# Kernel tuning notes

Measured on AMD Instinct MI355X. Metric: run time of the kernel, lower is better.

The kernel has to match this reference:

```python
import jax, jax.numpy as jnp
import numpy as np

B, NS, NT = 4, 512, 512
D_IN, C1, R, C2 = 128, 64, 32, 32
E = 32768
STEPS = 10


def setup_inputs() -> dict:
    key = jax.random.key(0)
    ks = jax.random.split(key, 12)
    inp = {}
    inp['x_s'] = jax.random.normal(ks[0], (B * NS, D_IN), jnp.float32)
    inp['edge_index_s'] = jax.random.randint(ks[1], (2, E), 0, B * NS, jnp.int32)
    inp['edge_attr_s'] = jax.random.uniform(ks[2], (E,), jnp.float32)
    inp['batch_s'] = (jnp.arange(B * NS, dtype=jnp.int32) // NS)
    inp['x_t'] = jax.random.normal(ks[3], (B * NT, D_IN), jnp.float32)
    inp['edge_index_t'] = jax.random.randint(ks[4], (2, E), 0, B * NT, jnp.int32)
    inp['edge_attr_t'] = jax.random.uniform(ks[5], (E,), jnp.float32)
    inp['batch_t'] = (jnp.arange(B * NT, dtype=jnp.int32) // NT)
    inp['W1'] = jax.random.normal(ks[6], (D_IN, C1), jnp.float32) / np.float32(np.sqrt(D_IN))
    inp['W2'] = jax.random.normal(ks[7], (R, C2), jnp.float32) / np.float32(np.sqrt(R))
    inp['mw1'] = jax.random.normal(ks[8], (C2, C2), jnp.float32) / np.float32(np.sqrt(C2))
    inp['mb1'] = jnp.zeros((C2,), jnp.float32)
    inp['mw2'] = jax.random.normal(ks[9], (C2, 1), jnp.float32) / np.float32(np.sqrt(C2))
    inp['mb2'] = jnp.zeros((1,), jnp.float32)
    inp['r'] = jax.random.normal(ks[10], (STEPS, B, NS, R), jnp.float32)
    return inp


def psi(x, src, dst, ea, W, n):
    # simple message-passing GNN: edge-weighted neighbor aggregation + linear + ReLU
    m = jax.ops.segment_sum(x[src] * ea[:, None], dst, num_segments=n)
    return jax.nn.relu((x + m) @ W)


def reference(x_s, edge_index_s, edge_attr_s, batch_s, x_t, edge_index_t, edge_attr_t,
              batch_t, W1, W2, mw1, mb1, mw2, mb2, r):
    # Uniform graph sizes -> to_dense_batch is a reshape and all masks are True,
    # so masked_softmax reduces to plain softmax; batch_s/batch_t kept for interface fidelity.
    ss, ds = edge_index_s[0], edge_index_s[1]
    st, dt = edge_index_t[0], edge_index_t[1]
    h_s = psi(x_s, ss, ds, edge_attr_s, W1, B * NS).reshape(B, NS, C1)
    h_t = psi(x_t, st, dt, edge_attr_t, W1, B * NT).reshape(B, NT, C1)
    S_hat0 = jnp.einsum('bsc,btc->bst', h_s, h_t)  # [B, NS, NT]
    S_0 = jax.nn.softmax(S_hat0, axis=-1)

    def step(S_hat, r_i):
        S = jax.nn.softmax(S_hat, axis=-1)
        r_t = jnp.einsum('bst,bsr->btr', S, r_i)  # S^T @ r_s
        o_s = psi(r_i.reshape(B * NS, R), ss, ds, edge_attr_s, W2, B * NS).reshape(B, NS, C2)
        o_t = psi(r_t.reshape(B * NT, R), st, dt, edge_attr_t, W2, B * NT).reshape(B, NT, C2)
        Dm = o_s[:, :, None, :] - o_t[:, None, :, :]  # [B, NS, NT, C2] outer difference
        upd = (jax.nn.relu(Dm @ mw1 + mb1) @ mw2 + mb2)[..., 0]
        return S_hat + upd, None

    S_hat, _ = jax.lax.scan(step, S_hat0, r)
    S_L = jax.nn.softmax(S_hat, axis=-1)
    return (S_0, S_L)
```

## Files before the change

### kernel.cpp

```cpp
#include <hip/hip_runtime.h>


constexpr int kB = 4;
constexpr int kNS = 512;
constexpr int kNT = 512;
constexpr int kDin = 128;
constexpr int kC1 = 64;
constexpr int kR = 32;
constexpr int kC2 = 32;
constexpr int kE = 32768;
constexpr int kSteps = 10;
constexpr int kN = kB * kNS;
constexpr int kChunkStride = kR * kN;

__global__ void k_hist(const int* __restrict__ ei_s, const int* __restrict__ ei_t,
                       int* __restrict__ deg) {
  int g = blockIdx.y;
  const int* dst = (g ? ei_t : ei_s) + kE;
  int e = blockIdx.x * 256 + threadIdx.x;
  atomicAdd(&deg[g * kN + dst[e]], 1);
}

__global__ void k_scan(const int* __restrict__ deg, int* __restrict__ off,
                       int* __restrict__ cur) {
  int g = blockIdx.x;
  const int* d = deg + g * kN;
  int* o = off + g * (kN + 1);
  int* c = cur + g * kN;
  __shared__ int sums[256];
  int tid = threadIdx.x;
  int loc[8];
  int s = 0;
#pragma unroll
  for (int i = 0; i < 8; ++i) { loc[i] = d[tid * 8 + i]; s += loc[i]; }
  sums[tid] = s;
  __syncthreads();
  for (int st = 1; st < 256; st <<= 1) {
    int v = (tid >= st) ? sums[tid - st] : 0;
    __syncthreads();
    sums[tid] += v;
    __syncthreads();
  }
  int base = (tid > 0) ? sums[tid - 1] : 0;
#pragma unroll
  for (int i = 0; i < 8; ++i) {
    int idx = tid * 8 + i;
    o[idx] = base;
    c[idx] = base;
    base += loc[i];
  }
  if (tid == 255) o[kN] = base;
}

__global__ void k_scatter(const int* __restrict__ ei_s, const int* __restrict__ ei_t,
                          const float* __restrict__ ea_s, const float* __restrict__ ea_t,
                          int* __restrict__ cur, int* __restrict__ srcs,
                          float* __restrict__ eaw) {
  int g = blockIdx.y;
  const int* ei = g ? ei_t : ei_s;
  const float* ea = g ? ea_t : ea_s;
  int e = blockIdx.x * 256 + threadIdx.x;
  int d = ei[kE + e];
  int srcv = ei[e];
  int pos = atomicAdd(&cur[g * kN + d], 1);
  srcs[g * kE + pos] = srcv;
  eaw[g * kE + pos] = ea[e];
}

__global__ __launch_bounds__(128) void k_psi1(
    const float* __restrict__ x_s, const float* __restrict__ x_t,
    const int* __restrict__ srcs, const float* __restrict__ eaw,
    const int* __restrict__ off, const float* __restrict__ W1, float* __restrict__ h) {
  int g = blockIdx.y;
  const float* x = g ? x_t : x_s;
  const int* sr = srcs + g * kE;
  const float* ew = eaw + g * kE;
  const int* o = off + g * (kN + 1);
  float* ho = h + (size_t)g * kN * kC1;
  int n = blockIdx.x, f = threadIdx.x;
  __shared__ float y[kDin];
  int beg = o[n], end = o[n + 1];
  float m = 0.f;
  for (int idx = beg; idx < end; ++idx)
    m += x[(size_t)sr[idx] * kDin + f] * ew[idx];
  y[f] = x[(size_t)n * kDin + f] + m;
  __syncthreads();
  if (f < kC1) {
    float acc = 0.f;
#pragma unroll 16
    for (int k = 0; k < kDin; ++k) acc += y[k] * W1[k * kC1 + f];
    ho[(size_t)n * kC1 + f] = fmaxf(acc, 0.f);
  }
}

__global__ __launch_bounds__(256) void k_shat0(const float* __restrict__ h,
                                               float* __restrict__ Shat,
                                               float* __restrict__ pstatm,
                                               float* __restrict__ pstatl) {
  int b = blockIdx.z, s0 = blockIdx.y * 64, t0 = blockIdx.x * 64;
  const float* hs = h + (size_t)(b * kNS + s0) * kC1;
  const float* ht = h + (size_t)kN * kC1 + (size_t)(b * kNT + t0) * kC1;
  __shared__ float As[64 * 68];
  __shared__ float Bs[64 * 68];
  int tid = threadIdx.x;
#pragma unroll
  for (int k2 = 0; k2 < 4; ++k2) {
    int idx = tid + k2 * 256;
    int row = idx >> 4, c4 = idx & 15;
    float4 va = *(const float4*)(hs + (size_t)row * kC1 + c4 * 4);
    *(float4*)&As[row * 68 + c4 * 4] = va;
    float4 vb = *(const float4*)(ht + (size_t)row * kC1 + c4 * 4);
    *(float4*)&Bs[row * 68 + c4 * 4] = vb;
  }
  __syncthreads();
  int ts = tid >> 4, tt = tid & 15;
  float acc[4][4] = {};
#pragma unroll
  for (int cc = 0; cc < 16; ++cc) {
    float4 a[4], bt[4];
#pragma unroll
    for (int i = 0; i < 4; ++i) a[i] = *(const float4*)&As[(ts * 4 + i) * 68 + cc * 4];
#pragma unroll
    for (int k = 0; k < 4; ++k) bt[k] = *(const float4*)&Bs[(tt + 16 * k) * 68 + cc * 4];
#pragma unroll
    for (int i = 0; i < 4; ++i)
#pragma unroll
      for (int k = 0; k < 4; ++k)
        acc[i][k] += a[i].x * bt[k].x + a[i].y * bt[k].y + a[i].z * bt[k].z + a[i].w * bt[k].w;
  }
#pragma unroll
  for (int i = 0; i < 4; ++i) {
    int s = s0 + ts * 4 + i;
    float* row = Shat + (size_t)(b * kNS + s) * kNT;
#pragma unroll
    for (int k = 0; k < 4; ++k) row[t0 + tt + 16 * k] = acc[i][k];
  }
#pragma unroll
  for (int i = 0; i < 4; ++i) {
    float mm = fmaxf(fmaxf(acc[i][0], acc[i][1]), fmaxf(acc[i][2], acc[i][3]));
#pragma unroll
    for (int o2 = 8; o2; o2 >>= 1) mm = fmaxf(mm, __shfl_xor(mm, o2, 64));
    float se = 0.f;
#pragma unroll
    for (int k = 0; k < 4; ++k) se += __expf(acc[i][k] - mm);
#pragma unroll
    for (int o2 = 8; o2; o2 >>= 1) se += __shfl_xor(se, o2, 64);
    if (tt == 0) {
      int grow = b * kNS + s0 + ts * 4 + i;
      pstatm[blockIdx.x * kN + grow] = mm;
      pstatl[blockIdx.x * kN + grow] = se;
    }
  }
}

__global__ __launch_bounds__(256) void k_rt(const float* __restrict__ Shat,
                                            const float* __restrict__ pstatm,
                                            const float* __restrict__ pstatl,
                                            const float* __restrict__ ri,
                                            float* __restrict__ part, int nc,
                                            float* __restrict__ Sout) {
  int b = blockIdx.z, cs = blockIdx.y, s0 = cs * 64, t0 = blockIdx.x * 32;
  __shared__ float Wt[64 * 32];
  __shared__ float rch[64 * 32];
  __shared__ float lm[64], ll[64];
  int tid = threadIdx.x;
  if (tid < 64) {
    int row = b * kNS + s0 + tid;
    float m = -3.4e38f;
    for (int c = 0; c < nc; ++c) m = fmaxf(m, pstatm[c * kN + row]);
    float l = 0.f;
    for (int c = 0; c < nc; ++c) l += __expf(pstatm[c * kN + row] - m) * pstatl[c * kN + row];
    lm[tid] = m;
    ll[tid] = 1.f / l;
  }
  __syncthreads();
#pragma unroll
  for (int k2 = 0; k2 < 2; ++k2) {
    int idx = tid + k2 * 256;
    int row = idx >> 3, c4 = idx & 7;
    int grow = b * kNS + s0 + row;
    float4 v = *(const float4*)(Shat + (size_t)grow * kNT + t0 + c4 * 4);
    float m = lm[row], l = ll[row];
    float4 wv;
    wv.x = __expf(v.x - m) * l;
    wv.y = __expf(v.y - m) * l;
    wv.z = __expf(v.z - m) * l;
    wv.w = __expf(v.w - m) * l;
    *(float4*)&Wt[row * 32 + c4 * 4] = wv;
    if (Sout) *(float4*)(Sout + (size_t)grow * kNT + t0 + c4 * 4) = wv;
    float4 rv = *(const float4*)(ri + (size_t)grow * kR + c4 * 4);
    *(float4*)&rch[row * 32 + c4 * 4] = rv;
  }
  __syncthreads();
  int t_l = tid & 31, jg = tid >> 5;
  float4 acc = make_float4(0.f, 0.f, 0.f, 0.f);
  for (int s = 0; s < 64; ++s) {
    float wv = Wt[s * 32 + t_l];
    float4 rv = *(const float4*)&rch[s * 32 + jg * 4];
    acc.x += wv * rv.x; acc.y += wv * rv.y; acc.z += wv * rv.z; acc.w += wv * rv.w;
  }
  int gcol = b * kNT + t0 + t_l;
  *(float4*)&part[(size_t)cs * kChunkStride + (size_t)gcol * kR + jg * 4] = acc;
}

__device__ __forceinline__ void psi2_node(
    int n, const float* __restrict__ vin, const int* __restrict__ sr,
    const float* __restrict__ ew, const int* __restrict__ o,
    const float* __restrict__ W2, const float* __restrict__ mw1,
    const float* __restrict__ mb1, float* __restrict__ Pout) {
  int lane = threadIdx.x & 63;
  int f = lane & 31, hh = lane >> 5;
  int beg = o[n], end = o[n + 1];
  float m = 0.f;
  for (int idx = beg + hh; idx < end; idx += 2)
    m += vin[(size_t)sr[idx] * kR + f] * ew[idx];
  m += __shfl_down(m, 32, 64);
  float v = vin[(size_t)n * kR + f] + m;
  float acc = 0.f;
#pragma unroll
  for (int k = 0; k < kC2; ++k) acc += __shfl(v, k, 64) * W2[k * kC2 + f];
  float ov = fmaxf(acc, 0.f);
  float p = mb1 ? mb1[f] : 0.f;
#pragma unroll
  for (int k = 0; k < kC2; ++k) p += __shfl(ov, k, 64) * mw1[k * kC2 + f];
  if (lane < 32) Pout[(size_t)n * kC2 + f] = p;
}

__global__ __launch_bounds__(256) void k_psi2s(
    const float* __restrict__ r, const int* __restrict__ srcs,
    const float* __restrict__ eaw, const int* __restrict__ off,
    const float* __restrict__ W2, const float* __restrict__ mw1,
    const float* __restrict__ mb1, float* __restrict__ PsAll) {
  int nn = blockIdx.x * 4 + (threadIdx.x >> 6);
  int step = nn >> 11, node = nn & (kN - 1);
  psi2_node(node, r + (size_t)step * kN * kR, srcs, eaw, off, W2, mw1, mb1,
            PsAll + (size_t)step * kN * kR);
}

__global__ __launch_bounds__(256) void k_psi2t(
    const float* __restrict__ part, const int* __restrict__ srcs,
    const float* __restrict__ eaw, const int* __restrict__ off,
    const float* __restrict__ W2, const float* __restrict__ mw1,
    float* __restrict__ Pt) {
  int n = blockIdx.x * 4 + (threadIdx.x >> 6);
  int lane = threadIdx.x & 63;
  int f = lane & 31, hh = lane >> 5;
  const int* sr = srcs + kE;
  const float* ew = eaw + kE;
  const int* o = off + (kN + 1);
  int beg = o[n], end = o[n + 1];
  float m = 0.f;
  for (int idx = beg + hh; idx < end; idx += 2) {
    int rr = sr[idx];
    float v = 0.f;
#pragma unroll
    for (int cs = 0; cs < 8; ++cs) v += part[(size_t)cs * kChunkStride + (size_t)rr * kR + f];
    m += v * ew[idx];
  }
  m += __shfl_down(m, 32, 64);
  float vown = 0.f;
#pragma unroll
  for (int cs = 0; cs < 8; ++cs) vown += part[(size_t)cs * kChunkStride + (size_t)n * kR + f];
  float v = vown + m;
  float acc = 0.f;
#pragma unroll
  for (int k = 0; k < kC2; ++k) acc += __shfl(v, k, 64) * W2[k * kC2 + f];
  float ov = fmaxf(acc, 0.f);
  float p = 0.f;
#pragma unroll
  for (int k = 0; k < kC2; ++k) p += __shfl(ov, k, 64) * mw1[k * kC2 + f];
  if (lane < 32) Pt[(size_t)n * kC2 + f] = p;
}

__global__ __launch_bounds__(256) void k_upd(
    float* __restrict__ Shat, const float* __restrict__ Ps,
    const float* __restrict__ Pt, const float* __restrict__ mw2,
    const float* __restrict__ mb2, float* __restrict__ pstatm,
    float* __restrict__ pstatl) {
  __shared__ float pts[256 * 33];
  __shared__ float red[8 * 4];
  __shared__ float lmx[8];
  int tid = threadIdx.x;
  int g0 = blockIdx.x * 8;
  int cc = blockIdx.y;
  int bb = g0 >> 9;
  int c0 = cc * 256;
  const float4* PtB = (const float4*)(Pt + ((size_t)bb * kNT + c0) * kC2);
#pragma unroll
  for (int k = 0; k < 8; ++k) {
    int idx = tid + k * 256;
    int col = idx >> 3, q = idx & 7;
    float4 v = PtB[idx];
    float* d = &pts[col * 33 + q * 4];
    d[0] = v.x; d[1] = v.y; d[2] = v.z; d[3] = v.w;
  }
  __syncthreads();
  float pt[32];
#pragma unroll
  for (int j = 0; j < 32; ++j) pt[j] = pts[tid * 33 + j];
  float bias = mb2[0];
  float nv[8];
#pragma unroll
  for (int s = 0; s < 8; ++s) {
    const float* psr = Ps + (size_t)(g0 + s) * kC2;
    float u = 0.f;
#pragma unroll
    for (int j = 0; j < 32; ++j) u += fmaxf(psr[j] - pt[j], 0.f) * mw2[j];
    float* p = Shat + (size_t)(g0 + s) * kNT + c0 + tid;
    float v = *p + u + bias;
    *p = v;
    nv[s] = v;
  }
  int wv = tid >> 6, ln = tid & 63;
#pragma unroll
  for (int s = 0; s < 8; ++s) {
    float m = nv[s];
#pragma unroll
    for (int o2 = 32; o2; o2 >>= 1) m = fmaxf(m, __shfl_down(m, o2, 64));
    if (ln == 0) red[s * 4 + wv] = m;
  }
  __syncthreads();
  if (tid < 8) {
    lmx[tid] = fmaxf(fmaxf(red[tid * 4], red[tid * 4 + 1]),
                     fmaxf(red[tid * 4 + 2], red[tid * 4 + 3]));
  }
  __syncthreads();
#pragma unroll
  for (int s = 0; s < 8; ++s) {
    float e = __expf(nv[s] - lmx[s]);
#pragma unroll
    for (int o2 = 32; o2; o2 >>= 1) e += __shfl_down(e, o2, 64);
    if (ln == 0) red[s * 4 + wv] = e;
  }
  __syncthreads();
  if (tid < 8) {
    float l = red[tid * 4] + red[tid * 4 + 1] + red[tid * 4 + 2] + red[tid * 4 + 3];
    pstatm[cc * kN + g0 + tid] = lmx[tid];
    pstatl[cc * kN + g0 + tid] = l;
  }
}

__global__ __launch_bounds__(256) void k_out(const float* __restrict__ Shat,
                                             const float* __restrict__ pstatm,
                                             const float* __restrict__ pstatl,
                                             float* __restrict__ out) {
  int row = blockIdx.x, tid = threadIdx.x;
  float m0 = pstatm[row], m1 = pstatm[kN + row];
  float l0 = pstatl[row], l1 = pstatl[kN + row];
  float m = fmaxf(m0, m1);
  float linv = 1.f / (__expf(m0 - m) * l0 + __expf(m1 - m) * l1);
  const float* p = Shat + (size_t)row * kNT;
  float* d = out + (size_t)row * kNT;
  d[tid] = __expf(p[tid] - m) * linv;
  d[tid + 256] = __expf(p[tid + 256] - m) * linv;
}

extern "C" void kernel_launch(void* const* d_in, const int* in_sizes, int n_in,
                              void* d_out, int out_size, void* d_ws, size_t ws_size,
                              hipStream_t stream) {
  (void)in_sizes; (void)n_in; (void)out_size; (void)ws_size;
  const float* x_s = (const float*)d_in[0];
  const int* ei_s = (const int*)d_in[1];
  const float* ea_s = (const float*)d_in[2];
  const float* x_t = (const float*)d_in[4];
  const int* ei_t = (const int*)d_in[5];
  const float* ea_t = (const float*)d_in[6];
  const float* W1 = (const float*)d_in[8];
  const float* W2 = (const float*)d_in[9];
  const float* mw1 = (const float*)d_in[10];
  const float* mb1 = (const float*)d_in[11];
  const float* mw2 = (const float*)d_in[12];
  const float* mb2 = (const float*)d_in[13];
  const float* r = (const float*)d_in[14];
  float* out = (float*)d_out;

  char* w = (char*)d_ws;
  auto alloc = [&](size_t bytes) -> void* {
    void* p = (void*)w;
    w += (bytes + 255) & ~(size_t)255;
    return p;
  };
  int* deg = (int*)alloc((size_t)2 * kN * 4);
  int* off = (int*)alloc((size_t)2 * (kN + 1) * 4);
  int* cur = (int*)alloc((size_t)2 * kN * 4);
  int* srcs = (int*)alloc((size_t)2 * kE * 4);
  float* eaw = (float*)alloc((size_t)2 * kE * 4);
  float* h = (float*)alloc((size_t)2 * kN * kC1 * 4);
  float* Shat = (float*)alloc((size_t)kB * kNS * kNT * 4);
  float* pstatm = (float*)alloc((size_t)8 * kN * 4);
  float* pstatl = (float*)alloc((size_t)8 * kN * 4);
  float* PsAll = (float*)alloc((size_t)kSteps * kN * kR * 4);
  float* Pt = (float*)alloc((size_t)kN * kC2 * 4);
  float* part = (float*)alloc((size_t)8 * kChunkStride * 4);

  hipMemsetAsync(deg, 0, (size_t)2 * kN * 4, stream);
  k_hist<<<dim3(kE / 256, 2), 256, 0, stream>>>(ei_s, ei_t, deg);
  k_scan<<<2, 256, 0, stream>>>(deg, off, cur);
  k_scatter<<<dim3(kE / 256, 2), 256, 0, stream>>>(ei_s, ei_t, ea_s, ea_t, cur, srcs, eaw);
  k_psi2s<<<kSteps * kN / 4, 256, 0, stream>>>(r, srcs, eaw, off, W2, mw1, mb1, PsAll);
  k_psi1<<<dim3(kN, 2), 128, 0, stream>>>(x_s, x_t, srcs, eaw, off, W1, h);
  k_shat0<<<dim3(8, 8, kB), 256, 0, stream>>>(h, Shat, pstatm, pstatl);
  k_rt<<<dim3(16, 8, kB), 256, 0, stream>>>(Shat, pstatm, pstatl, r, part, 8, out);
  for (int i = 0; i < kSteps; ++i) {
    k_psi2t<<<kN / 4, 256, 0, stream>>>(part, srcs, eaw, off, W2, mw1, Pt);
    k_upd<<<dim3(kN / 8, 2), 256, 0, stream>>>(Shat, PsAll + (size_t)i * kN * kR, Pt,
                                               mw2, mb2, pstatm, pstatl);
    if (i + 1 < kSteps) {
      k_rt<<<dim3(16, 8, kB), 256, 0, stream>>>(Shat, pstatm, pstatl,
                                                r + (size_t)(i + 1) * kN * kR, part,
                                                2, nullptr);
    }
  }
  k_out<<<kN, 256, 0, stream>>>(Shat, pstatm, pstatl, out + (size_t)kB * kNS * kNT);
}
```

Before: 523.5 us.

## Widen k_rt tiles and add a separate partial-sum reduction before psi2t

```diff
diff --git a/kernel.cpp b/kernel.cpp
--- a/kernel.cpp
+++ b/kernel.cpp
@@ -159,8 +159,8 @@
                                             const float* __restrict__ ri,
                                             float* __restrict__ part, int nc,
                                             float* __restrict__ Sout) {
-  int b = blockIdx.z, cs = blockIdx.y, s0 = cs * 64, t0 = blockIdx.x * 32;
-  __shared__ float Wt[64 * 32];
+  int b = blockIdx.z, cs = blockIdx.y, s0 = cs * 64, t0 = blockIdx.x * 64;
+  __shared__ float Wt[64 * 64];
   __shared__ float rch[64 * 32];
   __shared__ float lm[64], ll[64];
   int tid = threadIdx.x;
@@ -175,9 +175,9 @@
   }
   __syncthreads();
 #pragma unroll
-  for (int k2 = 0; k2 < 2; ++k2) {
+  for (int k2 = 0; k2 < 4; ++k2) {
     int idx = tid + k2 * 256;
-    int row = idx >> 3, c4 = idx & 7;
+    int row = idx >> 4, c4 = idx & 15;
     int grow = b * kNS + s0 + row;
     float4 v = *(const float4*)(Shat + (size_t)grow * kNT + t0 + c4 * 4);
     float m = lm[row], l = ll[row];
@@ -186,21 +186,40 @@
     wv.y = __expf(v.y - m) * l;
     wv.z = __expf(v.z - m) * l;
     wv.w = __expf(v.w - m) * l;
-    *(float4*)&Wt[row * 32 + c4 * 4] = wv;
+    *(float4*)&Wt[row * 64 + c4 * 4] = wv;
     if (Sout) *(float4*)(Sout + (size_t)grow * kNT + t0 + c4 * 4) = wv;
-    float4 rv = *(const float4*)(ri + (size_t)grow * kR + c4 * 4);
-    *(float4*)&rch[row * 32 + c4 * 4] = rv;
-  }
-  __syncthreads();
-  int t_l = tid & 31, jg = tid >> 5;
-  float4 acc = make_float4(0.f, 0.f, 0.f, 0.f);
+  }
+#pragma unroll
+  for (int k2 = 0; k2 < 2; ++k2) {
+    int idx = tid + k2 * 256;
+    int row = idx >> 3, c4 = idx & 7;
+    float4 v = *(const float4*)(ri + (size_t)(b * kNS + s0 + row) * kR + c4 * 4);
+    *(float4*)&rch[row * 32 + c4 * 4] = v;
+  }
+  __syncthreads();
+  int t_l = tid & 63, jg = tid >> 6;
+  float acc[8] = {};
   for (int s = 0; s < 64; ++s) {
-    float wv = Wt[s * 32 + t_l];
-    float4 rv = *(const float4*)&rch[s * 32 + jg * 4];
-    acc.x += wv * rv.x; acc.y += wv * rv.y; acc.z += wv * rv.z; acc.w += wv * rv.w;
+    float wv = Wt[s * 64 + t_l];
+    float4 ra = *(const float4*)&rch[s * 32 + jg * 8];
+    float4 rb = *(const float4*)&rch[s * 32 + jg * 8 + 4];
+    acc[0] += wv * ra.x; acc[1] += wv * ra.y; acc[2] += wv * ra.z; acc[3] += wv * ra.w;
+    acc[4] += wv * rb.x; acc[5] += wv * rb.y; acc[6] += wv * rb.z; acc[7] += wv * rb.w;
   }
   int gcol = b * kNT + t0 + t_l;
-  *(float4*)&part[(size_t)cs * kChunkStride + (size_t)gcol * kR + jg * 4] = acc;
+  float* dst = part + (size_t)cs * kChunkStride + (size_t)jg * 8 * kN + gcol;
+#pragma unroll
+  for (int q = 0; q < 8; ++q) dst[(size_t)q * kN] = acc[q];
+}
+
+__global__ __launch_bounds__(256) void k_red(const float* __restrict__ part,
+                                             float* __restrict__ rt) {
+  int idx = blockIdx.x * 256 + threadIdx.x;
+  int j = idx >> 11, col = idx & (kN - 1);
+  float s = 0.f;
+#pragma unroll
+  for (int cs = 0; cs < 8; ++cs) s += part[(size_t)cs * kChunkStride + idx];
+  rt[(size_t)col * kR + j] = s;
 }
 
 __device__ __forceinline__ void psi2_node(
@@ -238,38 +257,12 @@
 }
 
 __global__ __launch_bounds__(256) void k_psi2t(
-    const float* __restrict__ part, const int* __restrict__ srcs,
+    const float* __restrict__ rt, const int* __restrict__ srcs,
     const float* __restrict__ eaw, const int* __restrict__ off,
     const float* __restrict__ W2, const float* __restrict__ mw1,
     float* __restrict__ Pt) {
   int n = blockIdx.x * 4 + (threadIdx.x >> 6);
-  int lane = threadIdx.x & 63;
-  int f = lane & 31, hh = lane >> 5;
-  const int* sr = srcs + kE;
-  const float* ew = eaw + kE;
-  const int* o = off + (kN + 1);
-  int beg = o[n], end = o[n + 1];
-  float m = 0.f;
-  for (int idx = beg + hh; idx < end; idx += 2) {
-    int rr = sr[idx];
-    float v = 0.f;
-#pragma unroll
-    for (int cs = 0; cs < 8; ++cs) v += part[(size_t)cs * kChunkStride + (size_t)rr * kR + f];
-    m += v * ew[idx];
-  }
-  m += __shfl_down(m, 32, 64);
-  float vown = 0.f;
-#pragma unroll
-  for (int cs = 0; cs < 8; ++cs) vown += part[(size_t)cs * kChunkStride + (size_t)n * kR + f];
-  float v = vown + m;
-  float acc = 0.f;
-#pragma unroll
-  for (int k = 0; k < kC2; ++k) acc += __shfl(v, k, 64) * W2[k * kC2 + f];
-  float ov = fmaxf(acc, 0.f);
-  float p = 0.f;
-#pragma unroll
-  for (int k = 0; k < kC2; ++k) p += __shfl(ov, k, 64) * mw1[k * kC2 + f];
-  if (lane < 32) Pt[(size_t)n * kC2 + f] = p;
+  psi2_node(n, rt, srcs + kE, eaw + kE, off + (kN + 1), W2, mw1, nullptr, Pt);
 }
 
 __global__ __launch_bounds__(256) void k_upd(
@@ -389,6 +382,7 @@
   float* Shat = (float*)alloc((size_t)kB * kNS * kNT * 4);
   float* pstatm = (float*)alloc((size_t)8 * kN * 4);
   float* pstatl = (float*)alloc((size_t)8 * kN * 4);
+  float* rt = (float*)alloc((size_t)kN * kR * 4);
   float* PsAll = (float*)alloc((size_t)kSteps * kN * kR * 4);
   float* Pt = (float*)alloc((size_t)kN * kC2 * 4);
   float* part = (float*)alloc((size_t)8 * kChunkStride * 4);
@@ -400,15 +394,17 @@
   k_psi2s<<<kSteps * kN / 4, 256, 0, stream>>>(r, srcs, eaw, off, W2, mw1, mb1, PsAll);
   k_psi1<<<dim3(kN, 2), 128, 0, stream>>>(x_s, x_t, srcs, eaw, off, W1, h);
   k_shat0<<<dim3(8, 8, kB), 256, 0, stream>>>(h, Shat, pstatm, pstatl);
-  k_rt<<<dim3(16, 8, kB), 256, 0, stream>>>(Shat, pstatm, pstatl, r, part, 8, out);
+  k_rt<<<dim3(8, 8, kB), 256, 0, stream>>>(Shat, pstatm, pstatl, r, part, 8, out);
+  k_red<<<kChunkStride / 256, 256, 0, stream>>>(part, rt);
   for (int i = 0; i < kSteps; ++i) {
-    k_psi2t<<<kN / 4, 256, 0, stream>>>(part, srcs, eaw, off, W2, mw1, Pt);
+    k_psi2t<<<kN / 4, 256, 0, stream>>>(rt, srcs, eaw, off, W2, mw1, Pt);
     k_upd<<<dim3(kN / 8, 2), 256, 0, stream>>>(Shat, PsAll + (size_t)i * kN * kR, Pt,
                                                mw2, mb2, pstatm, pstatl);
     if (i + 1 < kSteps) {
-      k_rt<<<dim3(16, 8, kB), 256, 0, stream>>>(Shat, pstatm, pstatl,
-                                                r + (size_t)(i + 1) * kN * kR, part,
-                                                2, nullptr);
+      k_rt<<<dim3(8, 8, kB), 256, 0, stream>>>(Shat, pstatm, pstatl,
+                                               r + (size_t)(i + 1) * kN * kR, part,
+                                               2, nullptr);
+      k_red<<<kChunkStride / 256, 256, 0, stream>>>(part, rt);
     }
   }
   k_out<<<kN, 256, 0, stream>>>(Shat, pstatm, pstatl, out + (size_t)kB * kNS * kNT);
```

After: 486.4 us. -7.1%, faster.
